# Performance work log

Measured on AMD Instinct MI355X. Metric: run time of the kernel, lower is better.

## Reference

```python
import jax, jax.numpy as jnp
import numpy as np


def setup_inputs() -> dict:
    key = jax.random.key(0)
    ks = jax.random.split(key, 6)
    B, H, W, C = 8, 128, 128, 256
    x = jax.random.normal(ks[0], (B, H, W), dtype=jnp.float32)
    atten_x_full = jax.random.normal(ks[1], (B, H, W, W), dtype=jnp.float32)
    atten_y_full = jax.random.normal(ks[2], (B, W, H, H), dtype=jnp.float32)
    value_full = jax.random.normal(ks[3], (B, H, W, C), dtype=jnp.float32)
    # nn.Parameter init: shift = |randn|, bias = -|randn|
    shift = jnp.abs(jax.random.normal(ks[4], (1,), dtype=jnp.float32))
    bias = -jnp.abs(jax.random.normal(ks[5], (1,), dtype=jnp.float32))
    return {"x": x, "atten_x_full": atten_x_full, "atten_y_full": atten_y_full,
            "value_full": value_full, "shift": shift, "bias": bias}


def reference(x, atten_x_full, atten_y_full, value_full, shift, bias):
    H, W = x.shape[1], x.shape[2]
    # Gaussian distance biases: gx[c, h] = -(shift*(h-c)^2 + bias), gy[r, w] likewise
    hw = jnp.arange(W, dtype=jnp.float32)
    hh = jnp.arange(H, dtype=jnp.float32)
    gx = -(shift[0] * (hw[None, :] - hw[:, None]) ** 2 + bias[0])  # [W, W]
    gy = -(shift[0] * (hh[None, :] - hh[:, None]) ** 2 + bias[0])  # [H, H]
    # atten_x_full indexed [b, r, c, k] -> add gx[c, k]; softmax over k (row direction)
    Ax = jax.nn.softmax(atten_x_full + gx[None, None, :, :], axis=-1)  # [B,H,W,W]
    # atten_y_full indexed [b, c, r, k] -> add gy[r, k]; softmax over k (col direction)
    Ay = jax.nn.softmax(atten_y_full + gy[None, None, :, :], axis=-1)  # [B,W,H,H]
    out = (jnp.einsum('brck,brkd->brcd', Ax, value_full)
           + jnp.einsum('bcrk,bkcd->brcd', Ay, value_full))  # [B,H,W,C]
    return out
```

## Files before the change

kernel.cpp:

```cpp
#include <hip/hip_runtime.h>

typedef __attribute__((ext_vector_type(8))) short short8;
typedef __attribute__((ext_vector_type(4))) float floatx4;
typedef _Float16 half4 __attribute__((ext_vector_type(4)));

#define LDK 136
#define LDS_BYTES (256 * LDK * 2)
#define OUT_ELEMS (8LL * 128 * 128 * 256)

__device__ __forceinline__ unsigned f2bf1(float x) {
    unsigned u = __builtin_bit_cast(unsigned, x);
    return (u + 0x7fffu + ((u >> 16) & 1u)) >> 16;
}
__device__ __forceinline__ unsigned packbf(float lo, float hi) {
    return f2bf1(lo) | (f2bf1(hi) << 16);
}

template <int MODE>
__global__ __launch_bounds__(512, 4) void gtrans(
    const float* __restrict__ atten, const float* __restrict__ value,
    float* __restrict__ out, _Float16* __restrict__ ws,
    const float* __restrict__ shiftp, const float* __restrict__ biasp,
    int s0, int s1)
{
    extern __shared__ short Buf[];
    unsigned* Buf32 = (unsigned*)Buf;

    const int bi   = blockIdx.x;
    const int b    = bi >> 7;
    const int i    = bi & 127;
    const int tid  = threadIdx.x;
    const int lane = tid & 63;
    const int w    = tid >> 6;

    const float shift = shiftp[0];
    const float bias  = biasp[0];

    const size_t obase_off = (size_t)b * (128 * 128 * 256) + (size_t)i * s0;
    const float* abase = atten + (size_t)bi * (128 * 128);
    const float* vbase = value + obase_off;

    const int rrow = 16 * w + (lane & 15);
    const int kq8  = (lane >> 4) * 8;
    const int k0   = 16 * w + 2 * (lane >> 3);
    const int d0   = 4 * (lane & 7);
    const int am   = lane & 15;
    const int dq   = 4 * (lane >> 4);

    floatx4 aA[8];
#pragma unroll
    for (int ks = 0; ks < 4; ++ks) {
        const float* ap = abase + rrow * 128 + ks * 32 + kq8;
        aA[2 * ks]     = __builtin_nontemporal_load((const floatx4*)(ap));
        aA[2 * ks + 1] = __builtin_nontemporal_load((const floatx4*)(ap + 4));
    }
    floatx4 va[8], vb[8];
    {
        const float* vp0 = vbase + (size_t)k0 * s1 + d0;
        const float* vp1 = vp0 + s1;
#pragma unroll
        for (int q = 0; q < 8; ++q) va[q] = *(const floatx4*)(vp0 + 32 * q);
#pragma unroll
        for (int q = 0; q < 8; ++q) vb[q] = *(const floatx4*)(vp1 + 32 * q);
    }

    short8 bfrag[4];
    {
        floatx4 e8[8];
        float mx = -1e30f;
#pragma unroll
        for (int j = 0; j < 8; ++j) {
            const int kb = (j >> 1) * 32 + kq8 + (j & 1) * 4;
            floatx4 v = aA[j], t;
#pragma unroll
            for (int e = 0; e < 4; ++e) {
                float d = (float)(kb + e - rrow);
                t[e] = v[e] - (shift * d * d + bias);
            }
            e8[j] = t;
            mx = fmaxf(mx, fmaxf(fmaxf(t[0], t[1]), fmaxf(t[2], t[3])));
        }
        mx = fmaxf(mx, __shfl_xor(mx, 16, 64));
        mx = fmaxf(mx, __shfl_xor(mx, 32, 64));
        float ssum = 0.0f;
#pragma unroll
        for (int j = 0; j < 8; ++j) {
            floatx4 t = e8[j];
#pragma unroll
            for (int e = 0; e < 4; ++e) t[e] = __expf(t[e] - mx);
            e8[j] = t;
            ssum += (t[0] + t[1]) + (t[2] + t[3]);
        }
        ssum += __shfl_xor(ssum, 16, 64);
        ssum += __shfl_xor(ssum, 32, 64);
        float r = 1.0f / ssum;
#pragma unroll
        for (int ks = 0; ks < 4; ++ks) {
            union { short8 s; unsigned u[4]; } uu;
            floatx4 lo = e8[2 * ks], hi = e8[2 * ks + 1];
            uu.u[0] = packbf(lo[0] * r, lo[1] * r);
            uu.u[1] = packbf(lo[2] * r, lo[3] * r);
            uu.u[2] = packbf(hi[0] * r, hi[1] * r);
            uu.u[3] = packbf(hi[2] * r, hi[3] * r);
            bfrag[ks] = uu.s;
        }
    }

#pragma unroll
    for (int q = 0; q < 8; ++q)
#pragma unroll
        for (int e = 0; e < 4; ++e)
            Buf32[(d0 + 32 * q + e) * (LDK / 2) + (k0 >> 1)] = packbf(va[q][e], vb[q][e]);

    __builtin_amdgcn_sched_barrier(0);
    asm volatile("s_waitcnt lgkmcnt(0)" ::: "memory");
    __builtin_amdgcn_s_barrier();

    float*     orow = out + obase_off + (size_t)rrow * s1 + dq;
    _Float16*  wrow = ws  + obase_off + (size_t)rrow * s1 + dq;
#pragma unroll
    for (int g = 0; g < 4; ++g) {
        floatx4 acc[4];
        if (MODE == 2) {
#pragma unroll
            for (int t = 0; t < 4; ++t)
                acc[t] = *(const floatx4*)(orow + g * 64 + t * 16);
        } else if (MODE == 3) {
#pragma unroll
            for (int t = 0; t < 4; ++t) {
                half4 h = *(const half4*)(wrow + g * 64 + t * 16);
                floatx4 f;
#pragma unroll
                for (int e = 0; e < 4; ++e) f[e] = (float)h[e];
                acc[t] = f;
            }
        } else {
#pragma unroll
            for (int t = 0; t < 4; ++t) acc[t] = (floatx4)0.0f;
        }
#pragma unroll
        for (int tt = 0; tt < 4; ++tt) {
            const short* base = &Buf[((g * 4 + tt) * 16 + am) * LDK + kq8];
#pragma unroll
            for (int ks = 0; ks < 4; ++ks) {
                short8 af = *(const short8*)(base + ks * 32);
                acc[tt] = __builtin_amdgcn_mfma_f32_16x16x32_bf16(af, bfrag[ks], acc[tt], 0, 0, 0);
            }
        }
#pragma unroll
        for (int t = 0; t < 4; ++t) {
            if (MODE == 1) {
                half4 h;
#pragma unroll
                for (int e = 0; e < 4; ++e) h[e] = (_Float16)acc[t][e];
                *(half4*)(wrow + g * 64 + t * 16) = h;
            } else if (MODE == 3) {
                __builtin_nontemporal_store(acc[t], (floatx4*)(orow + g * 64 + t * 16));
            } else {
                *(floatx4*)(orow + g * 64 + t * 16) = acc[t];
            }
        }
    }
}

extern "C" void kernel_launch(void* const* d_in, const int* in_sizes, int n_in,
                              void* d_out, int out_size, void* d_ws, size_t ws_size,
                              hipStream_t stream) {
    const float* atten_x = (const float*)d_in[1];
    const float* atten_y = (const float*)d_in[2];
    const float* value   = (const float*)d_in[3];
    const float* shiftp  = (const float*)d_in[4];
    const float* biasp   = (const float*)d_in[5];
    float* out = (float*)d_out;
    _Float16* ws = (_Float16*)d_ws;

    static bool inited = false;
    if (!inited) {
        hipFuncSetAttribute((const void*)&gtrans<0>, hipFuncAttributeMaxDynamicSharedMemorySize, LDS_BYTES);
        hipFuncSetAttribute((const void*)&gtrans<1>, hipFuncAttributeMaxDynamicSharedMemorySize, LDS_BYTES);
        hipFuncSetAttribute((const void*)&gtrans<2>, hipFuncAttributeMaxDynamicSharedMemorySize, LDS_BYTES);
        hipFuncSetAttribute((const void*)&gtrans<3>, hipFuncAttributeMaxDynamicSharedMemorySize, LDS_BYTES);
        inited = true;
    }

    const bool use_ws = (ws != nullptr) && (ws_size >= (size_t)OUT_ELEMS * sizeof(_Float16));

    dim3 grid(1024), block(512);
    if (use_ws) {
        gtrans<1><<<grid, block, LDS_BYTES, stream>>>(atten_x, value, out, ws, shiftp, biasp,
                                                      128 * 256, 256);
        gtrans<3><<<grid, block, LDS_BYTES, stream>>>(atten_y, value, out, ws, shiftp, biasp,
                                                      256, 128 * 256);
    } else {
        gtrans<0><<<grid, block, LDS_BYTES, stream>>>(atten_x, value, out, ws, shiftp, biasp,
                                                      128 * 256, 256);
        gtrans<2><<<grid, block, LDS_BYTES, stream>>>(atten_y, value, out, ws, shiftp, biasp,
                                                      256, 128 * 256);
    }
}
```

Baseline: 365.4 us.

## Split value staging into two halves to halve LDS and double occupancy

The value tile staged in LDS now covers 128 output channels at a time instead of 256, processed in two passes with a barrier between them. This halves the dynamic LDS per block and lowers register pressure (fewer value registers, softmax computed in place in aA), and launch bounds are raised to 8 blocks per CU to exploit that. The trade-off is an extra barrier and serialized load-then-compute per half, which limits overlap within a block.

```diff
diff --git a/kernel.cpp b/kernel.cpp
--- a/kernel.cpp
+++ b/kernel.cpp
@@ -5,7 +5,7 @@
 typedef _Float16 half4 __attribute__((ext_vector_type(4)));
 
 #define LDK 136
-#define LDS_BYTES (256 * LDK * 2)
+#define LDS_BYTES (128 * LDK * 2)
 #define OUT_ELEMS (8LL * 128 * 128 * 256)
 
 __device__ __forceinline__ unsigned f2bf1(float x) {
@@ -17,7 +17,7 @@
 }
 
 template <int MODE>
-__global__ __launch_bounds__(512, 4) void gtrans(
+__global__ __launch_bounds__(512, 8) void gtrans(
     const float* __restrict__ atten, const float* __restrict__ value,
     float* __restrict__ out, _Float16* __restrict__ ws,
     const float* __restrict__ shiftp, const float* __restrict__ biasp,
@@ -40,12 +40,13 @@
     const float* abase = atten + (size_t)bi * (128 * 128);
     const float* vbase = value + obase_off;
 
-    const int rrow = 16 * w + (lane & 15);
-    const int kq8  = (lane >> 4) * 8;
-    const int k0   = 16 * w + 2 * (lane >> 3);
-    const int d0   = 4 * (lane & 7);
-    const int am   = lane & 15;
-    const int dq   = 4 * (lane >> 4);
+    const int rrow  = 16 * w + (lane & 15);
+    const int kq8   = (lane >> 4) * 8;
+    const int am    = lane & 15;
+    const int dq    = 4 * (lane >> 4);
+    const int k0    = 16 * w + 2 * (lane >> 3);
+    const int dl    = 4 * (lane & 7);
+    const int col32 = k0 >> 1;
 
     floatx4 aA[8];
 #pragma unroll
@@ -54,30 +55,20 @@
         aA[2 * ks]     = __builtin_nontemporal_load((const floatx4*)(ap));
         aA[2 * ks + 1] = __builtin_nontemporal_load((const floatx4*)(ap + 4));
     }
-    floatx4 va[8], vb[8];
-    {
-        const float* vp0 = vbase + (size_t)k0 * s1 + d0;
-        const float* vp1 = vp0 + s1;
-#pragma unroll
-        for (int q = 0; q < 8; ++q) va[q] = *(const floatx4*)(vp0 + 32 * q);
-#pragma unroll
-        for (int q = 0; q < 8; ++q) vb[q] = *(const floatx4*)(vp1 + 32 * q);
-    }
 
     short8 bfrag[4];
     {
-        floatx4 e8[8];
         float mx = -1e30f;
 #pragma unroll
         for (int j = 0; j < 8; ++j) {
             const int kb = (j >> 1) * 32 + kq8 + (j & 1) * 4;
-            floatx4 v = aA[j], t;
+            floatx4 t = aA[j];
 #pragma unroll
             for (int e = 0; e < 4; ++e) {
                 float d = (float)(kb + e - rrow);
-                t[e] = v[e] - (shift * d * d + bias);
-            }
-            e8[j] = t;
+                t[e] = t[e] - (shift * d * d + bias);
+            }
+            aA[j] = t;
             mx = fmaxf(mx, fmaxf(fmaxf(t[0], t[1]), fmaxf(t[2], t[3])));
         }
         mx = fmaxf(mx, __shfl_xor(mx, 16, 64));
@@ -85,10 +76,10 @@
         float ssum = 0.0f;
 #pragma unroll
         for (int j = 0; j < 8; ++j) {
-            floatx4 t = e8[j];
+            floatx4 t = aA[j];
 #pragma unroll
             for (int e = 0; e < 4; ++e) t[e] = __expf(t[e] - mx);
-            e8[j] = t;
+            aA[j] = t;
             ssum += (t[0] + t[1]) + (t[2] + t[3]);
         }
         ssum += __shfl_xor(ssum, 16, 64);
@@ -97,7 +88,7 @@
 #pragma unroll
         for (int ks = 0; ks < 4; ++ks) {
             union { short8 s; unsigned u[4]; } uu;
-            floatx4 lo = e8[2 * ks], hi = e8[2 * ks + 1];
+            floatx4 lo = aA[2 * ks], hi = aA[2 * ks + 1];
             uu.u[0] = packbf(lo[0] * r, lo[1] * r);
             uu.u[1] = packbf(lo[2] * r, lo[3] * r);
             uu.u[2] = packbf(hi[0] * r, hi[1] * r);
@@ -106,60 +97,76 @@
         }
     }
 
-#pragma unroll
-    for (int q = 0; q < 8; ++q)
-#pragma unroll
-        for (int e = 0; e < 4; ++e)
-            Buf32[(d0 + 32 * q + e) * (LDK / 2) + (k0 >> 1)] = packbf(va[q][e], vb[q][e]);
-
-    __builtin_amdgcn_sched_barrier(0);
-    asm volatile("s_waitcnt lgkmcnt(0)" ::: "memory");
-    __builtin_amdgcn_s_barrier();
-
-    float*     orow = out + obase_off + (size_t)rrow * s1 + dq;
-    _Float16*  wrow = ws  + obase_off + (size_t)rrow * s1 + dq;
-#pragma unroll
-    for (int g = 0; g < 4; ++g) {
-        floatx4 acc[4];
-        if (MODE == 2) {
-#pragma unroll
-            for (int t = 0; t < 4; ++t)
-                acc[t] = *(const floatx4*)(orow + g * 64 + t * 16);
-        } else if (MODE == 3) {
+    float*    orow = out + obase_off + (size_t)rrow * s1 + dq;
+    _Float16* wrow = ws  + obase_off + (size_t)rrow * s1 + dq;
+
+#pragma unroll
+    for (int half = 0; half < 2; ++half) {
+        floatx4 va[4], vb[4];
+        {
+            const float* vp0 = vbase + (size_t)k0 * s1 + half * 128 + dl;
+            const float* vp1 = vp0 + s1;
+#pragma unroll
+            for (int q = 0; q < 4; ++q) va[q] = *(const floatx4*)(vp0 + 32 * q);
+#pragma unroll
+            for (int q = 0; q < 4; ++q) vb[q] = *(const floatx4*)(vp1 + 32 * q);
+        }
+#pragma unroll
+        for (int q = 0; q < 4; ++q)
+#pragma unroll
+            for (int e = 0; e < 4; ++e)
+                Buf32[(dl + 32 * q + e) * (LDK / 2) + col32] = packbf(va[q][e], vb[q][e]);
+
+        __builtin_amdgcn_sched_barrier(0);
+        asm volatile("s_waitcnt lgkmcnt(0)" ::: "memory");
+        __builtin_amdgcn_s_barrier();
+
+#pragma unroll
+        for (int g = 0; g < 2; ++g) {
+            const int cb = half * 128 + g * 64;
+            floatx4 acc[4];
+            if (MODE == 2) {
+#pragma unroll
+                for (int t = 0; t < 4; ++t)
+                    acc[t] = *(const floatx4*)(orow + cb + t * 16);
+            } else if (MODE == 3) {
+#pragma unroll
+                for (int t = 0; t < 4; ++t) {
+                    half4 h = *(const half4*)(wrow + cb + t * 16);
+                    floatx4 f;
+#pragma unroll
+                    for (int e = 0; e < 4; ++e) f[e] = (float)h[e];
+                    acc[t] = f;
+                }
+            } else {
+#pragma unroll
+                for (int t = 0; t < 4; ++t) acc[t] = (floatx4)0.0f;
+            }
+#pragma unroll
+            for (int tt = 0; tt < 4; ++tt) {
+                const short* base = &Buf[((g * 4 + tt) * 16 + am) * LDK + kq8];
+#pragma unroll
+                for (int ks = 0; ks < 4; ++ks) {
+                    short8 af = *(const short8*)(base + ks * 32);
+                    acc[tt] = __builtin_amdgcn_mfma_f32_16x16x32_bf16(af, bfrag[ks], acc[tt], 0, 0, 0);
+                }
+            }
 #pragma unroll
             for (int t = 0; t < 4; ++t) {
-                half4 h = *(const half4*)(wrow + g * 64 + t * 16);
-                floatx4 f;
-#pragma unroll
-                for (int e = 0; e < 4; ++e) f[e] = (float)h[e];
-                acc[t] = f;
-            }
-        } else {
-#pragma unroll
-            for (int t = 0; t < 4; ++t) acc[t] = (floatx4)0.0f;
-        }
-#pragma unroll
-        for (int tt = 0; tt < 4; ++tt) {
-            const short* base = &Buf[((g * 4 + tt) * 16 + am) * LDK + kq8];
-#pragma unroll
-            for (int ks = 0; ks < 4; ++ks) {
-                short8 af = *(const short8*)(base + ks * 32);
-                acc[tt] = __builtin_amdgcn_mfma_f32_16x16x32_bf16(af, bfrag[ks], acc[tt], 0, 0, 0);
-            }
-        }
-#pragma unroll
-        for (int t = 0; t < 4; ++t) {
-            if (MODE == 1) {
-                half4 h;
-#pragma unroll
-                for (int e = 0; e < 4; ++e) h[e] = (_Float16)acc[t][e];
-                *(half4*)(wrow + g * 64 + t * 16) = h;
-            } else if (MODE == 3) {
-                __builtin_nontemporal_store(acc[t], (floatx4*)(orow + g * 64 + t * 16));
-            } else {
-                *(floatx4*)(orow + g * 64 + t * 16) = acc[t];
-            }
-        }
+                if (MODE == 1) {
+                    half4 h;
+#pragma unroll
+                    for (int e = 0; e < 4; ++e) h[e] = (_Float16)acc[t][e];
+                    *(half4*)(wrow + cb + t * 16) = h;
+                } else if (MODE == 3) {
+                    __builtin_nontemporal_store(acc[t], (floatx4*)(orow + cb + t * 16));
+                } else {
+                    *(floatx4*)(orow + cb + t * 16) = acc[t];
+                }
+            }
+        }
+        if (half == 0)
+            __builtin_amdgcn_s_barrier();
     }
 }
 
```

After: 363.9 us. No clear change (-0.4%).
